# Performance work log

Hardware: AMD Instinct MI355X
Metric: run time of the kernel (lower is better)

Reference implementation:

```python
import jax, jax.numpy as jnp
import numpy as np


def _lstm_cell(x, h, c, w_ih, w_hh, b_ih, b_hh):
    gates = x @ w_ih.T + b_ih + h @ w_hh.T + b_hh  # [B, 4H]
    i, f, g, o = jnp.split(gates, 4, axis=1)
    i = jax.nn.sigmoid(i)
    f = jax.nn.sigmoid(f)
    g = jnp.tanh(g)
    o = jax.nn.sigmoid(o)
    c_next = f * c + i * g
    h_next = o * jnp.tanh(c_next)
    return h_next, c_next


def setup_inputs() -> dict:
    key = jax.random.key(0)
    B, T, D_ENC, H, E, J, V = 32, 512, 512, 640, 640, 640, 4096
    ks = jax.random.split(key, 20)
    s = 0.05
    return {
        "encoder_outputs": jax.random.normal(ks[0], (B, D_ENC, T), jnp.float32),
        "targets": jax.random.randint(ks[1], (B, 1), 0, V, jnp.int64),
        "target_length": jnp.ones((B,), jnp.int32),
        "input_states_1": jax.random.normal(ks[2], (2, B, H), jnp.float32),
        "input_states_2": jax.random.normal(ks[3], (2, B, H), jnp.float32),
        "lstm_w_ih_l0": jax.random.normal(ks[4], (4 * H, E), jnp.float32) * s,
        "lstm_w_hh_l0": jax.random.normal(ks[5], (4 * H, H), jnp.float32) * s,
        "lstm_b_ih_l0": jax.random.normal(ks[6], (4 * H,), jnp.float32) * s,
        "lstm_b_hh_l0": jax.random.normal(ks[7], (4 * H,), jnp.float32) * s,
        "lstm_w_ih_l1": jax.random.normal(ks[8], (4 * H, H), jnp.float32) * s,
        "lstm_w_hh_l1": jax.random.normal(ks[9], (4 * H, H), jnp.float32) * s,
        "lstm_b_ih_l1": jax.random.normal(ks[10], (4 * H,), jnp.float32) * s,
        "lstm_b_hh_l1": jax.random.normal(ks[11], (4 * H,), jnp.float32) * s,
        "embed_weight": jax.random.normal(ks[12], (V, E), jnp.float32) * s,
        "joint_enc_weight": jax.random.normal(ks[13], (J, D_ENC), jnp.float32) * s,
        "joint_enc_bias": jax.random.normal(ks[14], (J,), jnp.float32) * s,
        "joint_pred_weight": jax.random.normal(ks[15], (J, H), jnp.float32) * s,
        "joint_pred_bias": jax.random.normal(ks[16], (J,), jnp.float32) * s,
        "joint_out_weight": jax.random.normal(ks[17], (V, J), jnp.float32) * s,
        "joint_out_bias": jax.random.normal(ks[18], (V,), jnp.float32) * s,
    }


def reference(encoder_outputs, targets, target_length, input_states_1, input_states_2,
              lstm_w_ih_l0, lstm_w_hh_l0, lstm_b_ih_l0, lstm_b_hh_l0,
              lstm_w_ih_l1, lstm_w_hh_l1, lstm_b_ih_l1, lstm_b_hh_l1,
              embed_weight, joint_enc_weight, joint_enc_bias,
              joint_pred_weight, joint_pred_bias, joint_out_weight, joint_out_bias):
    tokens = targets.astype(jnp.int64)
    x_t = embed_weight[tokens[:, 0]]  # [B, E] (only first token used)
    h0, c0 = _lstm_cell(x_t, input_states_1[0], input_states_2[0],
                        lstm_w_ih_l0, lstm_w_hh_l0, lstm_b_ih_l0, lstm_b_hh_l0)
    h1, c1 = _lstm_cell(h0, input_states_1[1], input_states_2[1],
                        lstm_w_ih_l1, lstm_w_hh_l1, lstm_b_ih_l1, lstm_b_hh_l1)
    enc = jnp.transpose(encoder_outputs, (0, 2, 1))  # [B, T, D_enc]
    f = enc @ joint_enc_weight.T + joint_enc_bias    # [B, T, J]
    g = h1 @ joint_pred_weight.T + joint_pred_bias   # [B, J] (U=1)
    joint = jax.nn.relu(f[:, :, None, :] + g[:, None, None, :])  # [B, T, 1, J]
    outputs = joint @ joint_out_weight.T + joint_out_bias        # [B, T, 1, V]
    output_states_1 = jnp.stack([h0, h1], axis=0)
    output_states_2 = jnp.stack([c0, c1], axis=0)
    return outputs, target_length, output_states_1, output_states_2
```

## Files before the change

### kernel.cpp

```cpp
#include <hip/hip_runtime.h>
#include <stdint.h>

#define B_  32
#define T_  512
#define DE_ 512
#define H_  640
#define V_  4096
#define J_  640

typedef __attribute__((ext_vector_type(4))) float  f32x4;
typedef __attribute__((ext_vector_type(8))) __bf16 bf16x8;

typedef __attribute__((address_space(3))) void LdsV;
typedef __attribute__((address_space(1))) void GloV;

__device__ __forceinline__ unsigned short f2bf(float f) {
    uint32_t u = __builtin_bit_cast(uint32_t, f);
    u += 0x7fffu + ((u >> 16) & 1u);
    return (unsigned short)(u >> 16);
}

__global__ void conv_f32_bf16_k(const float* __restrict__ src,
                                unsigned short* __restrict__ dst, int n) {
    int i = blockIdx.x * blockDim.x + threadIdx.x;
    if (i < n) dst[i] = f2bf(src[i]);
}

__global__ void enc_transpose_k(const float* __restrict__ enc,
                                unsigned short* __restrict__ out) {
    __shared__ float tile[32][33];
    int b  = blockIdx.z;
    int t0 = blockIdx.x * 32, d0 = blockIdx.y * 32;
    int tx = threadIdx.x & 31;
    int ty = (threadIdx.x >> 5) * 4;
    const float* src = enc + ((size_t)b * DE_ + d0) * T_ + t0;
#pragma unroll
    for (int i = 0; i < 4; i++)
        tile[ty + i][tx] = src[(size_t)(ty + i) * T_ + tx];
    __syncthreads();
    unsigned short* dst = out + ((size_t)b * T_ + t0) * DE_ + d0;
#pragma unroll
    for (int i = 0; i < 4; i++)
        dst[(size_t)(ty + i) * DE_ + tx] = f2bf(tile[tx][ty + i]);
}

__global__ void lstm_gates_k(const float* __restrict__ x, const int* __restrict__ tok,
                             const float* __restrict__ emb, const float* __restrict__ h,
                             const float* __restrict__ wih, const float* __restrict__ whh,
                             const float* __restrict__ bih, const float* __restrict__ bhh,
                             float* __restrict__ gates) {
    int n = blockIdx.x, lane = threadIdx.x;
    float wi[10], wh[10];
#pragma unroll
    for (int i = 0; i < 10; i++) {
        wi[i] = wih[(size_t)n * H_ + lane + 64 * i];
        wh[i] = whh[(size_t)n * H_ + lane + 64 * i];
    }
    float bias = bih[n] + bhh[n];
    for (int b = 0; b < B_; b++) {
        const float* xr = tok ? (emb + (size_t)tok[b] * H_) : (x + (size_t)b * H_);
        const float* hr = h + (size_t)b * H_;
        float s = 0.f;
#pragma unroll
        for (int i = 0; i < 10; i++)
            s += wi[i] * xr[lane + 64 * i] + wh[i] * hr[lane + 64 * i];
#pragma unroll
        for (int off = 32; off > 0; off >>= 1)
            s += __shfl_down(s, off, 64);
        if (lane == 0) gates[(size_t)b * (4 * H_) + n] = s + bias;
    }
}

__global__ void lstm_update_k(const float* __restrict__ gates, const float* __restrict__ c_in,
                              float* __restrict__ h_out, float* __restrict__ c_out,
                              const int* __restrict__ tlen, float* __restrict__ tlen_out) {
    int idx = blockIdx.x * blockDim.x + threadIdx.x;
    if (tlen_out != nullptr && idx < B_) tlen_out[idx] = (float)tlen[idx];
    if (idx >= B_ * H_) return;
    int b = idx / H_, j = idx - b * H_;
    const float* gr = gates + (size_t)b * 4 * H_;
    float ig = 1.f / (1.f + expf(-gr[j]));
    float fg = 1.f / (1.f + expf(-gr[H_ + j]));
    float gg = tanhf(gr[2 * H_ + j]);
    float og = 1.f / (1.f + expf(-gr[3 * H_ + j]));
    float c  = fg * c_in[idx] + ig * gg;
    h_out[idx] = og * tanhf(c);
    c_out[idx] = c;
}

__global__ void pred_g_k(const float* __restrict__ h1, const float* __restrict__ wp,
                         const float* __restrict__ bp, float* __restrict__ g) {
    int j = blockIdx.x, lane = threadIdx.x;
    float w[10];
#pragma unroll
    for (int i = 0; i < 10; i++) w[i] = wp[(size_t)j * H_ + lane + 64 * i];
    for (int b = 0; b < B_; b++) {
        const float* hr = h1 + (size_t)b * H_;
        float s = 0.f;
#pragma unroll
        for (int i = 0; i < 10; i++) s += w[i] * hr[lane + 64 * i];
#pragma unroll
        for (int off = 32; off > 0; off >>= 1)
            s += __shfl_down(s, off, 64);
        if (lane == 0) g[(size_t)b * J_ + j] = s + bp[j];
    }
}

template <int K, int EPI>
__global__ __launch_bounds__(256) void gemm_bt_k(
        const unsigned short* __restrict__ A, const unsigned short* __restrict__ Bm,
        const float* __restrict__ bias, const float* __restrict__ g,
        float* __restrict__ outF, unsigned short* __restrict__ outU, int ldn) {
    __shared__ __align__(16) unsigned short As[128 * 32];
    __shared__ __align__(16) unsigned short Bs[128 * 32];
    const int tid  = threadIdx.x;
    const int w    = tid >> 6;
    const int lane = tid & 63;
    const int tile_n = blockIdx.x * 128;
    const int tile_m = blockIdx.y * 128;
    const int wm = w & 1, wn = w >> 1;
    const int l15 = lane & 15, quad = lane >> 4;
    const int lr = lane >> 2, lc = lane & 3;

    f32x4 zero = {0.f, 0.f, 0.f, 0.f};
    f32x4 acc[4][4];
#pragma unroll
    for (int i = 0; i < 4; i++)
#pragma unroll
        for (int j = 0; j < 4; j++) acc[i][j] = zero;

    for (int k0 = 0; k0 < K; k0 += 32) {
#pragma unroll
        for (int cc = 0; cc < 2; cc++) {
            const int c = 2 * w + cc;
            const char* ga = (const char*)(A + (size_t)(tile_m + 16 * c + lr) * K)
                             + (size_t)k0 * 2 + lc * 16;
            __builtin_amdgcn_global_load_lds((const GloV*)ga,
                    (LdsV*)((char*)As + c * 1024), 16, 0, 0);
            const char* gb = (const char*)(Bm + (size_t)(tile_n + 16 * c + lr) * K)
                             + (size_t)k0 * 2 + lc * 16;
            __builtin_amdgcn_global_load_lds((const GloV*)gb,
                    (LdsV*)((char*)Bs + c * 1024), 16, 0, 0);
        }
        __syncthreads();

        bf16x8 av[4], bv[4];
#pragma unroll
        for (int i = 0; i < 4; i++) {
            av[i] = *(const bf16x8*)&As[(wm * 64 + i * 16 + l15) * 32 + quad * 8];
            bv[i] = *(const bf16x8*)&Bs[(wn * 64 + i * 16 + l15) * 32 + quad * 8];
        }
#pragma unroll
        for (int i = 0; i < 4; i++)
#pragma unroll
            for (int j = 0; j < 4; j++)
                acc[i][j] = __builtin_amdgcn_mfma_f32_16x16x32_bf16(av[i], bv[j], acc[i][j], 0, 0, 0);
        __syncthreads();
    }

#pragma unroll
    for (int i = 0; i < 4; i++) {
        const int mb = tile_m + wm * 64 + i * 16 + quad * 4;
#pragma unroll
        for (int j = 0; j < 4; j++) {
            const int n = tile_n + wn * 64 + j * 16 + l15;
#pragma unroll
            for (int r = 0; r < 4; r++) {
                float v = acc[i][j][r] + bias[n];
                if (EPI == 0) {
                    outF[(size_t)(mb + r) * ldn + n] = v;
                } else {
                    v += g[(size_t)((mb + r) >> 9) * J_ + n];
                    outU[(size_t)(mb + r) * ldn + n] = f2bf(fmaxf(v, 0.f));
                }
            }
        }
    }
}

extern "C" void kernel_launch(void* const* d_in, const int* in_sizes, int n_in,
                              void* d_out, int out_size, void* d_ws, size_t ws_size,
                              hipStream_t stream) {
    const float* enc   = (const float*)d_in[0];
    const int*   tgt   = (const int*)d_in[1];
    const int*   tlen  = (const int*)d_in[2];
    const float* st1   = (const float*)d_in[3];
    const float* st2   = (const float*)d_in[4];
    const float* wih0  = (const float*)d_in[5];
    const float* whh0  = (const float*)d_in[6];
    const float* bih0  = (const float*)d_in[7];
    const float* bhh0  = (const float*)d_in[8];
    const float* wih1  = (const float*)d_in[9];
    const float* whh1  = (const float*)d_in[10];
    const float* bih1  = (const float*)d_in[11];
    const float* bhh1  = (const float*)d_in[12];
    const float* emb   = (const float*)d_in[13];
    const float* wenc  = (const float*)d_in[14];
    const float* benc  = (const float*)d_in[15];
    const float* wpred = (const float*)d_in[16];
    const float* bpred = (const float*)d_in[17];
    const float* wout  = (const float*)d_in[18];
    const float* bout  = (const float*)d_in[19];

    float* out      = (float*)d_out;
    float* out_tlen = out + (size_t)B_ * T_ * V_;
    float* h0 = out_tlen + B_;
    float* h1 = h0 + B_ * H_;
    float* c0 = h1 + B_ * H_;
    float* c1 = c0 + B_ * H_;

    unsigned short* encB  = (unsigned short*)d_ws;
    unsigned short* pB    = encB + (size_t)B_ * T_ * DE_;
    unsigned short* woutB = pB + (size_t)B_ * T_ * J_;
    unsigned short* wencB = woutB + (size_t)V_ * J_;
    float* gates = (float*)(wencB + (size_t)J_ * DE_);
    float* gvec  = gates + B_ * 4 * H_;

    conv_f32_bf16_k<<<(V_ * J_ + 255) / 256, 256, 0, stream>>>(wout, woutB, V_ * J_);
    conv_f32_bf16_k<<<(J_ * DE_ + 255) / 256, 256, 0, stream>>>(wenc, wencB, J_ * DE_);
    enc_transpose_k<<<dim3(T_ / 32, DE_ / 32, B_), 256, 0, stream>>>(enc, encB);

    lstm_gates_k<<<4 * H_, 64, 0, stream>>>(nullptr, tgt, emb, st1, wih0, whh0, bih0, bhh0, gates);
    lstm_update_k<<<(B_ * H_ + 255) / 256, 256, 0, stream>>>(gates, st2, h0, c0, tlen, out_tlen);
    lstm_gates_k<<<4 * H_, 64, 0, stream>>>(h0, nullptr, nullptr, st1 + B_ * H_, wih1, whh1, bih1, bhh1, gates);
    lstm_update_k<<<(B_ * H_ + 255) / 256, 256, 0, stream>>>(gates, st2 + B_ * H_, h1, c1, nullptr, nullptr);
    pred_g_k<<<J_, 64, 0, stream>>>(h1, wpred, bpred, gvec);

    gemm_bt_k<DE_, 1><<<dim3(J_ / 128, (B_ * T_) / 128), 256, 0, stream>>>(
        encB, wencB, benc, gvec, nullptr, pB, J_);
    gemm_bt_k<J_, 0><<<dim3(V_ / 128, (B_ * T_) / 128), 256, 0, stream>>>(
        pB, woutB, bout, nullptr, out, nullptr, V_);
}
```

Baseline: 536.5 us.

## Fuse LSTM gate/update kernels, merge weight conversions, add 256x128 output GEMM

Fuses each LSTM layer's gate matvec and pointwise update into a single kernel that handles all four gates of one hidden unit per block, with the gate sums exchanged through shared memory. The two weight conversions are merged into one launch. The large output GEMM is replaced by a new kernel with 256x128 tiles, 512 threads, double-buffered direct global-to-LDS loads, and a block-index swizzle meant to improve L2 reuse. Together these cut launch count and aim to raise throughput on the dominant vocab GEMM, at the cost of more LDS per block and a more complex kernel.

```diff
diff --git a/kernel.cpp b/kernel.cpp
--- a/kernel.cpp
+++ b/kernel.cpp
@@ -20,10 +20,11 @@
     return (unsigned short)(u >> 16);
 }
 
-__global__ void conv_f32_bf16_k(const float* __restrict__ src,
-                                unsigned short* __restrict__ dst, int n) {
+__global__ void conv2_f32_bf16_k(const float* __restrict__ srcA, unsigned short* __restrict__ dstA, int nA,
+                                 const float* __restrict__ srcB, unsigned short* __restrict__ dstB, int nB) {
     int i = blockIdx.x * blockDim.x + threadIdx.x;
-    if (i < n) dst[i] = f2bf(src[i]);
+    if (i < nA) dstA[i] = f2bf(srcA[i]);
+    else if (i < nA + nB) dstB[i - nA] = f2bf(srcB[i - nA]);
 }
 
 __global__ void enc_transpose_k(const float* __restrict__ enc,
@@ -44,22 +45,27 @@
         dst[(size_t)(ty + i) * DE_ + tx] = f2bf(tile[tx][ty + i]);
 }
 
-__global__ void lstm_gates_k(const float* __restrict__ x, const int* __restrict__ tok,
-                             const float* __restrict__ emb, const float* __restrict__ h,
+__global__ void lstm_fused_k(const float* __restrict__ x, const int* __restrict__ tok,
+                             const float* __restrict__ emb, const float* __restrict__ h_in,
+                             const float* __restrict__ c_in,
                              const float* __restrict__ wih, const float* __restrict__ whh,
                              const float* __restrict__ bih, const float* __restrict__ bhh,
-                             float* __restrict__ gates) {
-    int n = blockIdx.x, lane = threadIdx.x;
+                             float* __restrict__ h_out, float* __restrict__ c_out,
+                             const int* __restrict__ tlen, float* __restrict__ tlen_out) {
+    const int j = blockIdx.x;
+    const int w = threadIdx.x >> 6, lane = threadIdx.x & 63;
+    const int n = w * H_ + j;
+    __shared__ float sm[4][B_];
     float wi[10], wh[10];
 #pragma unroll
     for (int i = 0; i < 10; i++) {
         wi[i] = wih[(size_t)n * H_ + lane + 64 * i];
         wh[i] = whh[(size_t)n * H_ + lane + 64 * i];
     }
-    float bias = bih[n] + bhh[n];
+    const float bias = bih[n] + bhh[n];
     for (int b = 0; b < B_; b++) {
         const float* xr = tok ? (emb + (size_t)tok[b] * H_) : (x + (size_t)b * H_);
-        const float* hr = h + (size_t)b * H_;
+        const float* hr = h_in + (size_t)b * H_;
         float s = 0.f;
 #pragma unroll
         for (int i = 0; i < 10; i++)
@@ -67,25 +73,20 @@
 #pragma unroll
         for (int off = 32; off > 0; off >>= 1)
             s += __shfl_down(s, off, 64);
-        if (lane == 0) gates[(size_t)b * (4 * H_) + n] = s + bias;
-    }
-}
-
-__global__ void lstm_update_k(const float* __restrict__ gates, const float* __restrict__ c_in,
-                              float* __restrict__ h_out, float* __restrict__ c_out,
-                              const int* __restrict__ tlen, float* __restrict__ tlen_out) {
-    int idx = blockIdx.x * blockDim.x + threadIdx.x;
-    if (tlen_out != nullptr && idx < B_) tlen_out[idx] = (float)tlen[idx];
-    if (idx >= B_ * H_) return;
-    int b = idx / H_, j = idx - b * H_;
-    const float* gr = gates + (size_t)b * 4 * H_;
-    float ig = 1.f / (1.f + expf(-gr[j]));
-    float fg = 1.f / (1.f + expf(-gr[H_ + j]));
-    float gg = tanhf(gr[2 * H_ + j]);
-    float og = 1.f / (1.f + expf(-gr[3 * H_ + j]));
-    float c  = fg * c_in[idx] + ig * gg;
-    h_out[idx] = og * tanhf(c);
-    c_out[idx] = c;
+        if (lane == 0) sm[w][b] = s + bias;
+    }
+    __syncthreads();
+    if (threadIdx.x < B_) {
+        const int b = threadIdx.x;
+        float ig = 1.f / (1.f + expf(-sm[0][b]));
+        float fg = 1.f / (1.f + expf(-sm[1][b]));
+        float gg = tanhf(sm[2][b]);
+        float og = 1.f / (1.f + expf(-sm[3][b]));
+        float c  = fg * c_in[(size_t)b * H_ + j] + ig * gg;
+        h_out[(size_t)b * H_ + j] = og * tanhf(c);
+        c_out[(size_t)b * H_ + j] = c;
+        if (tlen_out != nullptr && blockIdx.x == 0) tlen_out[b] = (float)tlen[b];
+    }
 }
 
 __global__ void pred_g_k(const float* __restrict__ h1, const float* __restrict__ wp,
@@ -176,6 +177,89 @@
             }
         }
     }
+}
+
+template <int M, int N, int K>
+__global__ __launch_bounds__(512, 4) void gemm_v3_k(
+        const unsigned short* __restrict__ A, const unsigned short* __restrict__ Bm,
+        const float* __restrict__ bias, float* __restrict__ out) {
+    __shared__ __align__(16) char lds[49152];
+    constexpr int NT  = K / 32;
+    constexpr int K2  = K * 2;
+    constexpr int NTN = N / 128;
+    constexpr int NWG = (M / 256) * NTN;
+
+    const int bid = blockIdx.x;
+    const int swz = (bid & 7) * (NWG / 8) + (bid >> 3);
+    const int tile_n = (swz % NTN) * 128;
+    const int tile_m = (swz / NTN) * 256;
+
+    const int tid  = threadIdx.x;
+    const int w    = tid >> 6;
+    const int l    = tid & 63;
+    const int wm   = w >> 1;
+    const int wn   = w & 1;
+    const int l15  = l & 15, quad = l >> 4;
+
+    const int ai0 = 2 * w, ai1 = 2 * w + 1;
+    const char* srcA0 = (const char*)A + (size_t)(tile_m + (ai0 >> 2) * 64 + l) * K2 + (ai0 & 3) * 16;
+    const char* srcA1 = (const char*)A + (size_t)(tile_m + (ai1 >> 2) * 64 + l) * K2 + (ai1 & 3) * 16;
+    const char* srcB  = (const char*)Bm + (size_t)(tile_n + (w >> 2) * 64 + l) * K2 + (w & 3) * 16;
+    const int dA0 = (ai0 & 3) * 4096 + (ai0 >> 2) * 1024;
+    const int dA1 = (ai1 & 3) * 4096 + (ai1 >> 2) * 1024;
+    const int dB  = 16384 + (w & 3) * 2048 + (w >> 2) * 1024;
+
+    auto stage = [&](int kt) {
+        char* base = lds + (kt & 1) * 24576;
+        const int kb = kt * 64;
+        __builtin_amdgcn_global_load_lds((const GloV*)(srcA0 + kb), (LdsV*)(base + dA0), 16, 0, 0);
+        __builtin_amdgcn_global_load_lds((const GloV*)(srcA1 + kb), (LdsV*)(base + dA1), 16, 0, 0);
+        __builtin_amdgcn_global_load_lds((const GloV*)(srcB  + kb), (LdsV*)(base + dB),  16, 0, 0);
+    };
+
+    const int aoff = quad * 4096 + (wm * 64 + l15) * 16;
+    const int boff = 16384 + quad * 2048 + (wn * 64 + l15) * 16;
+
+    f32x4 acc[4][4];
+    f32x4 zero = {0.f, 0.f, 0.f, 0.f};
+#pragma unroll
+    for (int i = 0; i < 4; i++)
+#pragma unroll
+        for (int j = 0; j < 4; j++) acc[i][j] = zero;
+
+    stage(0);
+    __syncthreads();
+
+    for (int t = 0; t < NT; ++t) {
+        if (t + 1 < NT) stage(t + 1);
+        const char* base = lds + (t & 1) * 24576;
+        bf16x8 av[4], bv[4];
+#pragma unroll
+        for (int i = 0; i < 4; i++) av[i] = *(const bf16x8*)(base + aoff + i * 256);
+#pragma unroll
+        for (int j = 0; j < 4; j++) bv[j] = *(const bf16x8*)(base + boff + j * 256);
+#pragma unroll
+        for (int i = 0; i < 4; i++)
+#pragma unroll
+            for (int j = 0; j < 4; j++)
+                acc[i][j] = __builtin_amdgcn_mfma_f32_16x16x32_bf16(av[i], bv[j], acc[i][j], 0, 0, 0);
+        __syncthreads();
+    }
+
+    const int cb = tile_n + wn * 64 + l15;
+    float bj[4];
+#pragma unroll
+    for (int j = 0; j < 4; j++) bj[j] = bias[cb + j * 16];
+    const int r0 = tile_m + wm * 64 + quad * 4;
+#pragma unroll
+    for (int i = 0; i < 4; i++)
+#pragma unroll
+        for (int r = 0; r < 4; r++) {
+            float* orow = out + (size_t)(r0 + i * 16 + r) * N;
+#pragma unroll
+            for (int j = 0; j < 4; j++)
+                orow[cb + j * 16] = acc[i][j][r] + bj[j];
+        }
 }
 
 extern "C" void kernel_launch(void* const* d_in, const int* in_sizes, int n_in,
@@ -213,21 +297,21 @@
     unsigned short* pB    = encB + (size_t)B_ * T_ * DE_;
     unsigned short* woutB = pB + (size_t)B_ * T_ * J_;
     unsigned short* wencB = woutB + (size_t)V_ * J_;
-    float* gates = (float*)(wencB + (size_t)J_ * DE_);
-    float* gvec  = gates + B_ * 4 * H_;
-
-    conv_f32_bf16_k<<<(V_ * J_ + 255) / 256, 256, 0, stream>>>(wout, woutB, V_ * J_);
-    conv_f32_bf16_k<<<(J_ * DE_ + 255) / 256, 256, 0, stream>>>(wenc, wencB, J_ * DE_);
+    float* gvec  = (float*)(wencB + (size_t)J_ * DE_);
+
+    conv2_f32_bf16_k<<<(V_ * J_ + J_ * DE_ + 255) / 256, 256, 0, stream>>>(
+        wout, woutB, V_ * J_, wenc, wencB, J_ * DE_);
     enc_transpose_k<<<dim3(T_ / 32, DE_ / 32, B_), 256, 0, stream>>>(enc, encB);
 
-    lstm_gates_k<<<4 * H_, 64, 0, stream>>>(nullptr, tgt, emb, st1, wih0, whh0, bih0, bhh0, gates);
-    lstm_update_k<<<(B_ * H_ + 255) / 256, 256, 0, stream>>>(gates, st2, h0, c0, tlen, out_tlen);
-    lstm_gates_k<<<4 * H_, 64, 0, stream>>>(h0, nullptr, nullptr, st1 + B_ * H_, wih1, whh1, bih1, bhh1, gates);
-    lstm_update_k<<<(B_ * H_ + 255) / 256, 256, 0, stream>>>(gates, st2 + B_ * H_, h1, c1, nullptr, nullptr);
+    lstm_fused_k<<<H_, 256, 0, stream>>>(nullptr, tgt, emb, st1, st2,
+                                         wih0, whh0, bih0, bhh0, h0, c0, tlen, out_tlen);
+    lstm_fused_k<<<H_, 256, 0, stream>>>(h0, nullptr, nullptr, st1 + B_ * H_, st2 + B_ * H_,
+                                         wih1, whh1, bih1, bhh1, h1, c1, nullptr, nullptr);
     pred_g_k<<<J_, 64, 0, stream>>>(h1, wpred, bpred, gvec);
 
     gemm_bt_k<DE_, 1><<<dim3(J_ / 128, (B_ * T_) / 128), 256, 0, stream>>>(
         encB, wencB, benc, gvec, nullptr, pB, J_);
-    gemm_bt_k<J_, 0><<<dim3(V_ / 128, (B_ * T_) / 128), 256, 0, stream>>>(
-        pB, woutB, bout, nullptr, out, nullptr, V_);
-}
+
+    gemm_v3_k<B_ * T_, V_, J_><<<dim3((B_ * T_ / 256) * (V_ / 128)), 512, 0, stream>>>(
+        pB, woutB, bout, out);
+}
```

Measured after the change: 571.4 us. +6.5%, slower.
